# Performance work log

Measured on AMD Instinct MI355X. Metric: run time of the kernel, lower is better.

The kernel has to match this reference:

```python
import jax, jax.numpy as jnp
import numpy as np

B, T, C = 32, 128, 64
E, H = 8, 4            # feat_dim, num_heads
D = E // H             # head_dim = 2
HID = 32               # hidden_dim


def setup_inputs() -> dict:
    key = jax.random.key(0)
    ks = jax.random.split(key, 20)
    s = 0.1
    return {
        "x": jax.random.normal(ks[0], (B, T, C), jnp.float32),
        # input_proj: Linear(C, C)
        "W_in": jax.random.normal(ks[1], (C, C), jnp.float32) * s,
        "b_in": jax.random.normal(ks[2], (C,), jnp.float32) * s,
        # time_step_score: Linear(C, C//4) -> GELU -> Linear(C//4, 1) -> Sigmoid
        "W_ts1": jax.random.normal(ks[3], (C // 4, C), jnp.float32) * s,
        "b_ts1": jax.random.normal(ks[4], (C // 4,), jnp.float32) * s,
        "W_ts2": jax.random.normal(ks[5], (1, C // 4), jnp.float32) * s,
        "b_ts2": jax.random.normal(ks[6], (1,), jnp.float32) * s,
        # per-channel GRU(1 -> E): torch gate order (r, z, n)
        "W_ih": jax.random.normal(ks[7], (C, 3 * E), jnp.float32) * s,      # input size 1
        "W_hh": jax.random.normal(ks[8], (C, 3 * E, E), jnp.float32) * s,
        "b_ih": jax.random.normal(ks[9], (C, 3 * E), jnp.float32) * s,
        "b_hh": jax.random.normal(ks[10], (C, 3 * E), jnp.float32) * s,
        # shared MultiheadAttention(E, 4): packed in_proj + out_proj
        "W_qkv": jax.random.normal(ks[11], (3 * E, E), jnp.float32) * s,
        "b_qkv": jax.random.normal(ks[12], (3 * E,), jnp.float32) * s,
        "W_o": jax.random.normal(ks[13], (E, E), jnp.float32) * s,
        "b_o": jax.random.normal(ks[14], (E,), jnp.float32) * s,
        # out_proj: Linear(C*E, HID)
        "W_out": jax.random.normal(ks[15], (HID, C * E), jnp.float32) * s,
        "b_out": jax.random.normal(ks[16], (HID,), jnp.float32) * s,
    }


def _forward(x, W_in, b_in, W_ts1, b_ts1, W_ts2, b_ts2,
             W_ih, W_hh, b_ih, b_hh, W_qkv, b_qkv, W_o, b_o, W_out, b_out):
    bs, ts, c = x.shape
    # time step importance: per-timestep MLP over the raw features
    h1 = jax.nn.gelu(jnp.einsum('btc,fc->btf', x, W_ts1) + b_ts1, approximate=False)
    ts_imp = jax.nn.sigmoid(jnp.einsum('btf,of->bto', h1, W_ts2) + b_ts2)[..., 0]  # [B,T]

    xp = jnp.einsum('btc,dc->btd', x, W_in) + b_in  # [B,T,C]

    # Batched per-channel GRU scan over time. state h: [B,C,E]
    def step(h, x_t):
        gi = x_t[:, :, None] * W_ih[None] + b_ih          # [B,C,3E]
        gh = jnp.einsum('bce,cge->bcg', h, W_hh) + b_hh   # [B,C,3E]
        ir, iz, inn = gi[..., :E], gi[..., E:2 * E], gi[..., 2 * E:]
        hr, hz, hn = gh[..., :E], gh[..., E:2 * E], gh[..., 2 * E:]
        r = jax.nn.sigmoid(ir + hr)
        z = jax.nn.sigmoid(iz + hz)
        n = jnp.tanh(inn + r * hn)
        h_new = (1.0 - z) * n + z * h
        return h_new, h_new

    h0 = jnp.zeros((bs, c, E), xp.dtype)
    _, hs = jax.lax.scan(step, h0, jnp.transpose(xp, (1, 0, 2)))  # [T,B,C,E]
    hs_bcte = jnp.transpose(hs, (1, 2, 0, 3))                     # [B,C,T,E]

    # Shared MHA applied independently per channel (batched over B*C)
    qkv = jnp.einsum('bcte,fe->bctf', hs_bcte, W_qkv) + b_qkv     # [B,C,T,3E]
    q, k, v = qkv[..., :E], qkv[..., E:2 * E], qkv[..., 2 * E:]
    def heads(t):
        return t.reshape(bs, c, ts, H, D)
    q, k, v = heads(q), heads(k), heads(v)
    scores = jnp.einsum('bcthd,bcshd->bchts', q, k) / np.sqrt(D)
    attn = jax.nn.softmax(scores, axis=-1)
    o = jnp.einsum('bchts,bcshd->bcthd', attn, v).reshape(bs, c, ts, E)
    attn_out = jnp.einsum('bcte,fe->bctf', o, W_o) + b_o          # [B,C,T,E]
    attention = jnp.transpose(attn_out, (0, 2, 1, 3))             # [B,T,C,E]

    out_flat = jnp.transpose(hs, (1, 0, 2, 3)).reshape(bs, ts, c * E)  # [B,T,C*E]
    out = jnp.einsum('btf,hf->bth', out_flat, W_out) + b_out           # [B,T,HID]

    feat_imp = jax.nn.sigmoid(attention.sum(axis=(1, 3)))   # [B,C]
    tsf_imp = jax.nn.sigmoid(attention.sum(axis=-1))        # [B,T,C]
    return out[:, -1, :], feat_imp, ts_imp, tsf_imp


def reference(x, W_in, b_in, W_ts1, b_ts1, W_ts2, b_ts2,
              W_ih, W_hh, b_ih, b_hh, W_qkv, b_qkv, W_o, b_o, W_out, b_out):
    return _forward(x, W_in, b_in, W_ts1, b_ts1, W_ts2, b_ts2,
                    W_ih, W_hh, b_ih, b_hh, W_qkv, b_qkv, W_o, b_o, W_out, b_out)
```

## Files before the change

kernel.cpp:

```cpp
#include <hip/hip_runtime.h>
#include <hip/hip_bf16.h>
#include <math.h>

#define B_ 32
#define T_ 128
#define C_ 64
#define E_ 8
#define HID_ 32

#define LOG2E 1.44269504088896341f

__device__ __forceinline__ float fast_rcp(float x) { return __builtin_amdgcn_rcpf(x); }
__device__ __forceinline__ float fast_exp2(float x) { return exp2f(x); }
__device__ __forceinline__ float fast_sigmoid(float x) {
    return fast_rcp(1.0f + fast_exp2(-LOG2E * x));
}
__device__ __forceinline__ float fast_tanh(float x) {
    float xc = __builtin_amdgcn_fmed3f(x, -15.0f, 15.0f);
    float t = fast_exp2(2.0f * LOG2E * xc);
    return (t - 1.0f) * fast_rcp(t + 1.0f);
}

template <int CTRL>
__device__ __forceinline__ float dppf(float v) {
    return __int_as_float(__builtin_amdgcn_update_dpp(
        __float_as_int(v), __float_as_int(v), CTRL, 0xF, 0xF, false));
}
#define QP_XOR1 0xB1
#define QP_XOR2 0x4E
#define QP_XOR3 0x1B
#define HALF_MIRROR 0x141

__global__ __launch_bounds__(64) void k_pre_ts(
    const float* __restrict__ x, const float* __restrict__ W_in, const float* __restrict__ b_in,
    const float* __restrict__ W_ts1, const float* __restrict__ b_ts1,
    const float* __restrict__ W_ts2, const float* __restrict__ b_ts2,
    float* __restrict__ xp, float* __restrict__ ts_imp)
{
    const int bt = blockIdx.x;
    const int tid = threadIdx.x;
    __shared__ __align__(16) float xs[C_];
    __shared__ float h1[16];
    if (tid < 16) ((float4*)xs)[tid] = ((const float4*)(x + bt * C_))[tid];
    __syncthreads();

    float a = b_in[tid];
    const float4* w4 = (const float4*)(W_in + tid * C_);
#pragma unroll
    for (int k4 = 0; k4 < 16; ++k4) {
        float4 xv = ((const float4*)xs)[k4];
        float4 wv = w4[k4];
        a = fmaf(xv.x, wv.x, a); a = fmaf(xv.y, wv.y, a);
        a = fmaf(xv.z, wv.z, a); a = fmaf(xv.w, wv.w, a);
    }
    xp[bt * C_ + tid] = a;

    if (tid < 16) {
        float s = b_ts1[tid];
#pragma unroll
        for (int k = 0; k < C_; ++k) s = fmaf(xs[k], W_ts1[tid * C_ + k], s);
        h1[tid] = 0.5f * s * (1.0f + erff(s * 0.70710678118654752f));
    }
    __syncthreads();
    if (tid == 0) {
        float s = b_ts2[0];
#pragma unroll
        for (int k = 0; k < 16; ++k) s = fmaf(h1[k], W_ts2[k], s);
        ts_imp[bt] = fast_sigmoid(s);
    }
}

__global__ __launch_bounds__(64) void k_gru(
    const float* __restrict__ xp, const float* __restrict__ W_ih, const float* __restrict__ W_hh,
    const float* __restrict__ b_ih, const float* __restrict__ b_hh,
    float* __restrict__ hs, float* __restrict__ fh)
{
    const int tid = threadIdx.x;
    const int ci = tid >> 3;
    const int e = tid & 7;
    const int chain = blockIdx.x * 8 + ci;
    const int c = chain & 63;

    __shared__ float xc[8][T_ + 1];

    const int c_base = (blockIdx.x & 7) * 8;
    const int bb = blockIdx.x >> 3;
    for (int idx = tid; idx < 8 * T_; idx += 64) {
        int cci = idx & 7, t = idx >> 3;
        xc[cci][t] = xp[(bb * T_ + t) * C_ + c_base + cci];
    }
    __syncthreads();

    float wr[8], wz[8], wn[8];
#pragma unroll
    for (int m = 0; m < 8; ++m) {
        const int j = e ^ m;
        wr[m] = W_hh[(c * 24 + 0  + e) * 8 + j];
        wz[m] = W_hh[(c * 24 + 8  + e) * 8 + j];
        wn[m] = W_hh[(c * 24 + 16 + e) * 8 + j];
    }
    const float wir = W_ih[c * 24 + e], wiz = W_ih[c * 24 + 8 + e], win = W_ih[c * 24 + 16 + e];
    const float cr = b_ih[c * 24 + e] + b_hh[c * 24 + e];
    const float cz = b_ih[c * 24 + 8 + e] + b_hh[c * 24 + 8 + e];
    const float bin_ = b_ih[c * 24 + 16 + e];
    const float bhn  = b_hh[c * 24 + 16 + e];

    float h = 0.0f;
    float* ho = hs + (size_t)chain * T_ * E_ + e;
    float xv = xc[ci][0];
    for (int t = 0; t < T_; ++t) {
        float xvn = xc[ci][t + 1];
        float p1 = dppf<QP_XOR1>(h);
        float p2 = dppf<QP_XOR2>(h);
        float p3 = dppf<QP_XOR3>(h);
        float p7 = dppf<HALF_MIRROR>(h);
        float p6 = dppf<HALF_MIRROR>(p1);
        float p5 = dppf<HALF_MIRROR>(p2);
        float p4 = dppf<HALF_MIRROR>(p3);
        const float pa[8] = {h, p1, p2, p3, p4, p5, p6, p7};

        float g0 = fmaf(pa[1], wr[1], pa[0] * wr[0]);
        float g1 = fmaf(pa[3], wr[3], pa[2] * wr[2]);
        float g2 = fmaf(pa[5], wr[5], pa[4] * wr[4]);
        float g3 = fmaf(pa[7], wr[7], pa[6] * wr[6]);
        float gr = fmaf(xv, wir, cr) + ((g0 + g1) + (g2 + g3));
        float z0 = fmaf(pa[1], wz[1], pa[0] * wz[0]);
        float z1 = fmaf(pa[3], wz[3], pa[2] * wz[2]);
        float z2 = fmaf(pa[5], wz[5], pa[4] * wz[4]);
        float z3 = fmaf(pa[7], wz[7], pa[6] * wz[6]);
        float gz = fmaf(xv, wiz, cz) + ((z0 + z1) + (z2 + z3));
        float n0 = fmaf(pa[1], wn[1], pa[0] * wn[0]);
        float n1 = fmaf(pa[3], wn[3], pa[2] * wn[2]);
        float n2 = fmaf(pa[5], wn[5], pa[4] * wn[4]);
        float n3 = fmaf(pa[7], wn[7], pa[6] * wn[6]);
        float hn = bhn + ((n0 + n1) + (n2 + n3));
        float gn = fmaf(xv, win, bin_);
        float r = fast_sigmoid(gr);
        float z = fast_sigmoid(gz);
        float nn = fast_tanh(fmaf(r, hn, gn));
        h = fmaf(z, h - nn, nn);
        ho[t * E_] = h;
        xv = xvn;
    }
    fh[chain * E_ + e] = h;
}

__global__ __launch_bounds__(128) void k_qkvu(
    const float* __restrict__ hs, const float* __restrict__ W_qkv, const float* __restrict__ b_qkv,
    const float* __restrict__ W_o,
    float* __restrict__ kub)
{
    const int bc = blockIdx.x;
    const int s = threadIdx.x;
    const float4* hp = (const float4*)(hs + (size_t)bc * T_ * E_ + s * E_);
    float4 h0 = hp[0], h1 = hp[1];
    float hr[E_] = {h0.x, h0.y, h0.z, h0.w, h1.x, h1.y, h1.z, h1.w};

    float kv[E_];
#pragma unroll
    for (int f = 0; f < E_; ++f) {
        float a = b_qkv[E_ + f];
#pragma unroll
        for (int j = 0; j < E_; ++j) a = fmaf(hr[j], W_qkv[(E_ + f) * E_ + j], a);
        kv[f] = a;
    }
    float ws[E_];
#pragma unroll
    for (int d = 0; d < E_; ++d) {
        float wv = 0.0f;
#pragma unroll
        for (int fp = 0; fp < E_; ++fp) wv += W_o[fp * E_ + d];
        ws[d] = wv;
    }
    float vv[E_];
#pragma unroll
    for (int f = 0; f < E_; ++f) {
        float a = b_qkv[2 * E_ + f];
#pragma unroll
        for (int j = 0; j < E_; ++j) a = fmaf(hr[j], W_qkv[(2 * E_ + f) * E_ + j], a);
        vv[f] = a;
    }
    float4 uu;
    uu.x = fmaf(vv[1], ws[1], vv[0] * ws[0]);
    uu.y = fmaf(vv[3], ws[3], vv[2] * ws[2]);
    uu.z = fmaf(vv[5], ws[5], vv[4] * ws[4]);
    uu.w = fmaf(vv[7], ws[7], vv[6] * ws[6]);

    float4* rec = (float4*)(kub + ((size_t)bc * T_ + s) * 12);
    rec[0] = make_float4(kv[0], kv[1], kv[2], kv[3]);
    rec[1] = make_float4(kv[4], kv[5], kv[6], kv[7]);
    rec[2] = uu;
}

__global__ __launch_bounds__(128) void k_attn2(
    const float* __restrict__ hs, const float* __restrict__ W_qkv, const float* __restrict__ b_qkv,
    const float* __restrict__ b_o, const float* __restrict__ kub,
    float* __restrict__ feat_imp, float* __restrict__ tsf_imp)
{
    const int bc = blockIdx.x;
    const int b = bc >> 6, c = bc & 63;
    const int tid = threadIdx.x;
    const int w = tid >> 6;
    const int lane = tid & 63;
    const int row = tid;

    __shared__ float red2[2];

    const float qscale = 0.70710678118654752f * LOG2E;

    float q[E_];
    {
        const float4* hp = (const float4*)(hs + (size_t)bc * T_ * E_ + row * E_);
        float4 h0 = hp[0], h1 = hp[1];
        float hr[E_] = {h0.x, h0.y, h0.z, h0.w, h1.x, h1.y, h1.z, h1.w};
#pragma unroll
        for (int f = 0; f < E_; ++f) {
            float a = b_qkv[f];
#pragma unroll
            for (int j = 0; j < E_; ++j) a = fmaf(hr[j], W_qkv[f * E_ + j], a);
            q[f] = a * qscale;
        }
    }

    const float* kbase = kub + (size_t)bc * T_ * 12;
    float l[4] = {0.f, 0.f, 0.f, 0.f};
    float S[4] = {0.f, 0.f, 0.f, 0.f};
#pragma unroll 4
    for (int s = 0; s < T_; ++s) {
        const float4* r4 = (const float4*)(kbase + (size_t)s * 12);
        float4 ka = r4[0];
        float4 kb4 = r4[1];
        float4 uu = r4[2];
        float p0 = fast_exp2(fmaf(q[1], ka.y, q[0] * ka.x));
        float p1 = fast_exp2(fmaf(q[3], ka.w, q[2] * ka.z));
        float p2 = fast_exp2(fmaf(q[5], kb4.y, q[4] * kb4.x));
        float p3 = fast_exp2(fmaf(q[7], kb4.w, q[6] * kb4.z));
        l[0] += p0; l[1] += p1; l[2] += p2; l[3] += p3;
        S[0] = fmaf(p0, uu.x, S[0]);
        S[1] = fmaf(p1, uu.y, S[1]);
        S[2] = fmaf(p2, uu.z, S[2]);
        S[3] = fmaf(p3, uu.w, S[3]);
    }

    float bsum = 0.0f;
#pragma unroll
    for (int fp = 0; fp < E_; ++fp) bsum += b_o[fp];
    float Sv = bsum;
#pragma unroll
    for (int hh = 0; hh < 4; ++hh) Sv = fmaf(S[hh], fast_rcp(l[hh]), Sv);

    tsf_imp[(size_t)b * T_ * C_ + (size_t)row * C_ + c] = fast_sigmoid(Sv);

    float fsum = Sv;
#pragma unroll
    for (int off = 1; off <= 32; off <<= 1) fsum += __shfl_xor(fsum, off);
    if (lane == 0) red2[w] = fsum;
    __syncthreads();
    if (tid == 0) feat_imp[bc] = fast_sigmoid(red2[0] + red2[1]);
}

__global__ __launch_bounds__(128) void k_attn(
    const float* __restrict__ hs, const float* __restrict__ W_qkv, const float* __restrict__ b_qkv,
    const float* __restrict__ W_o, const float* __restrict__ b_o,
    float* __restrict__ feat_imp, float* __restrict__ tsf_imp)
{
    const int bc = blockIdx.x;
    const int b = bc >> 6, c = bc & 63;
    const int tid = threadIdx.x;
    const int w = tid >> 6;
    const int lane = tid & 63;
    const int ri = lane >> 1;
    const int sh = lane & 1;
    const int row0 = w * 64 + ri;
    const int row1 = w * 64 + 32 + ri;

    __shared__ __align__(16) float ks[2][516];
    __shared__ __align__(16) float us[2][260];
    __shared__ float qsT[E_][T_];
    __shared__ float red2[2];

    const float qscale = 0.70710678118654752f * LOG2E;

    {
        const int srow = tid;
        const float4* hp = (const float4*)(hs + (size_t)bc * T_ * E_ + srow * E_);
        float4 h0 = hp[0], h1 = hp[1];
        float hr[E_] = {h0.x, h0.y, h0.z, h0.w, h1.x, h1.y, h1.z, h1.w};
        float* kdst = &ks[srow >> 6][(srow & 63) * 8];
        float kv[E_];
#pragma unroll
        for (int f = 0; f < E_; ++f) {
            float a = b_qkv[E_ + f];
#pragma unroll
            for (int j = 0; j < E_; ++j) a = fmaf(hr[j], W_qkv[(E_ + f) * E_ + j], a);
            kv[f] = a;
        }
        ((float4*)kdst)[0] = make_float4(kv[0], kv[1], kv[2], kv[3]);
        ((float4*)kdst)[1] = make_float4(kv[4], kv[5], kv[6], kv[7]);
#pragma unroll
        for (int f = 0; f < E_; ++f) {
            float a = b_qkv[f];
#pragma unroll
            for (int j = 0; j < E_; ++j) a = fmaf(hr[j], W_qkv[f * E_ + j], a);
            qsT[f][srow] = a * qscale;
        }
        float ws[E_];
#pragma unroll
        for (int d = 0; d < E_; ++d) {
            float wv = 0.0f;
#pragma unroll
            for (int fp = 0; fp < E_; ++fp) wv += W_o[fp * E_ + d];
            ws[d] = wv;
        }
        float vv[E_];
#pragma unroll
        for (int f = 0; f < E_; ++f) {
            float a = b_qkv[2 * E_ + f];
#pragma unroll
            for (int j = 0; j < E_; ++j) a = fmaf(hr[j], W_qkv[(2 * E_ + f) * E_ + j], a);
            vv[f] = a;
        }
        float4 uu;
        uu.x = fmaf(vv[1], ws[1], vv[0] * ws[0]);
        uu.y = fmaf(vv[3], ws[3], vv[2] * ws[2]);
        uu.z = fmaf(vv[5], ws[5], vv[4] * ws[4]);
        uu.w = fmaf(vv[7], ws[7], vv[6] * ws[6]);
        *((float4*)&us[srow >> 6][(srow & 63) * 4]) = uu;
    }
    __syncthreads();

    float q0[E_], q1[E_];
#pragma unroll
    for (int f = 0; f < E_; ++f) { q0[f] = qsT[f][row0]; q1[f] = qsT[f][row1]; }

    float l0[4] = {0.f,0.f,0.f,0.f}, S0[4] = {0.f,0.f,0.f,0.f};
    float l1[4] = {0.f,0.f,0.f,0.f}, S1[4] = {0.f,0.f,0.f,0.f};
    const float* kb = &ks[sh][0];
    const float* ub = &us[sh][0];
#pragma unroll 8
    for (int i = 0; i < 64; ++i) {
        float4 k0 = *(const float4*)(kb + i * 8);
        float4 k1 = *(const float4*)(kb + i * 8 + 4);
        float4 uu = *(const float4*)(ub + i * 4);
        float p00 = fast_exp2(fmaf(q0[1], k0.y, q0[0] * k0.x));
        float p01 = fast_exp2(fmaf(q0[3], k0.w, q0[2] * k0.z));
        float p02 = fast_exp2(fmaf(q0[5], k1.y, q0[4] * k1.x));
        float p03 = fast_exp2(fmaf(q0[7], k1.w, q0[6] * k1.z));
        float p10 = fast_exp2(fmaf(q1[1], k0.y, q1[0] * k0.x));
        float p11 = fast_exp2(fmaf(q1[3], k0.w, q1[2] * k0.z));
        float p12 = fast_exp2(fmaf(q1[5], k1.y, q1[4] * k1.x));
        float p13 = fast_exp2(fmaf(q1[7], k1.w, q1[6] * k1.z));
        l0[0] += p00; l0[1] += p01; l0[2] += p02; l0[3] += p03;
        l1[0] += p10; l1[1] += p11; l1[2] += p12; l1[3] += p13;
        S0[0] = fmaf(p00, uu.x, S0[0]); S0[1] = fmaf(p01, uu.y, S0[1]);
        S0[2] = fmaf(p02, uu.z, S0[2]); S0[3] = fmaf(p03, uu.w, S0[3]);
        S1[0] = fmaf(p10, uu.x, S1[0]); S1[1] = fmaf(p11, uu.y, S1[1]);
        S1[2] = fmaf(p12, uu.z, S1[2]); S1[3] = fmaf(p13, uu.w, S1[3]);
    }

#pragma unroll
    for (int i = 0; i < 4; ++i) {
        l0[i] += __shfl_xor(l0[i], 1);  S0[i] += __shfl_xor(S0[i], 1);
        l1[i] += __shfl_xor(l1[i], 1);  S1[i] += __shfl_xor(S1[i], 1);
    }

    float bsum = 0.0f;
#pragma unroll
    for (int fp = 0; fp < E_; ++fp) bsum += b_o[fp];
    float Sa = bsum, Sb = bsum;
#pragma unroll
    for (int hh = 0; hh < 4; ++hh) {
        Sa = fmaf(S0[hh], fast_rcp(l0[hh]), Sa);
        Sb = fmaf(S1[hh], fast_rcp(l1[hh]), Sb);
    }

    if (sh == 0) {
        tsf_imp[(size_t)b * T_ * C_ + (size_t)row0 * C_ + c] = fast_sigmoid(Sa);
        tsf_imp[(size_t)b * T_ * C_ + (size_t)row1 * C_ + c] = fast_sigmoid(Sb);
    }

    float fsum = Sa + Sb;
#pragma unroll
    for (int off = 2; off <= 32; off <<= 1) fsum += __shfl_xor(fsum, off);
    if (lane == 0) red2[w] = fsum;
    __syncthreads();
    if (tid == 0) feat_imp[bc] = fast_sigmoid(red2[0] + red2[1]);
}

__global__ __launch_bounds__(64) void k_out(
    const float* __restrict__ fh, const float* __restrict__ W_out, const float* __restrict__ b_out,
    float* __restrict__ out0)
{
    const int b = blockIdx.x;
    const int tid = threadIdx.x;
    __shared__ float hf[C_ * E_];
    const float4* src = (const float4*)(fh + (b * C_ + tid) * E_);
    float4* dst = (float4*)(hf + tid * E_);
    dst[0] = src[0];
    dst[1] = src[1];
    __syncthreads();
    if (tid < HID_) {
        float a = b_out[tid];
        const float* wo = W_out + tid * (C_ * E_);
        for (int k = 0; k < C_ * E_; ++k) a = fmaf(hf[k], wo[k], a);
        out0[b * HID_ + tid] = a;
    }
}

extern "C" void kernel_launch(void* const* d_in, const int* in_sizes, int n_in,
                              void* d_out, int out_size, void* d_ws, size_t ws_size,
                              hipStream_t stream) {
    (void)in_sizes; (void)n_in; (void)out_size;

    float* out0 = (float*)d_out;
    float* feat = out0 + B_ * HID_;
    float* tsim = feat + B_ * C_;
    float* tsf  = tsim + B_ * T_;

    const float* x     = (const float*)d_in[0];
    const float* W_in  = (const float*)d_in[1];
    const float* b_in  = (const float*)d_in[2];
    const float* W_ts1 = (const float*)d_in[3];
    const float* b_ts1 = (const float*)d_in[4];
    const float* W_ts2 = (const float*)d_in[5];
    const float* b_ts2 = (const float*)d_in[6];
    const float* W_ih  = (const float*)d_in[7];
    const float* W_hh  = (const float*)d_in[8];
    const float* b_ih  = (const float*)d_in[9];
    const float* b_hh  = (const float*)d_in[10];
    const float* W_qkv = (const float*)d_in[11];
    const float* b_qkv = (const float*)d_in[12];
    const float* W_o   = (const float*)d_in[13];
    const float* b_o   = (const float*)d_in[14];
    const float* W_out = (const float*)d_in[15];
    const float* b_out = (const float*)d_in[16];

    float* fhb = (float*)d_ws;
    float* xpb = fhb + B_ * C_ * E_;
    float* hsb = xpb + (size_t)B_ * T_ * C_;
    float* kub = hsb + (size_t)B_ * C_ * T_ * E_;

    const size_t need = ((size_t)B_ * C_ * E_ + (size_t)B_ * T_ * C_ +
                         (size_t)B_ * C_ * T_ * E_ + (size_t)B_ * C_ * T_ * 12) * 4;

    hipLaunchKernelGGL(k_pre_ts, dim3(B_ * T_), dim3(64), 0, stream,
                       x, W_in, b_in, W_ts1, b_ts1, W_ts2, b_ts2, xpb, tsim);
    hipLaunchKernelGGL(k_gru, dim3(B_ * C_ / 8), dim3(64), 0, stream,
                       xpb, W_ih, W_hh, b_ih, b_hh, hsb, fhb);
    hipLaunchKernelGGL(k_out, dim3(B_), dim3(64), 0, stream,
                       fhb, W_out, b_out, out0);

    if (ws_size >= need) {
        hipLaunchKernelGGL(k_qkvu, dim3(B_ * C_), dim3(128), 0, stream,
                           hsb, W_qkv, b_qkv, W_o, kub);
        hipLaunchKernelGGL(k_attn2, dim3(B_ * C_), dim3(128), 0, stream,
                           hsb, W_qkv, b_qkv, b_o, kub, feat, tsf);
    } else {
        hipLaunchKernelGGL(k_attn, dim3(B_ * C_), dim3(128), 0, stream,
                           hsb, W_qkv, b_qkv, W_o, b_o, feat, tsf);
    }
}
```

Measured before the change: 106.2 us.

## Split attention kernel across heads with one wave per head

The attention-summary kernel now launches 512 threads per (batch, channel) block, with each wave owning one head for 64 query rows instead of each thread handling all four heads. Per-head partial results go to shared memory and are summed by the first 128 threads before the sigmoid outputs and the feature reduction. This raises parallelism and cuts per-thread serial work in the 128-step key loop. In exchange it adds a shared-memory stage, an extra barrier, and scalar loads that re-read each record once per head.

```diff
diff --git a/kernel.cpp b/kernel.cpp
--- a/kernel.cpp
+++ b/kernel.cpp
@@ -192,7 +192,7 @@
     rec[2] = uu;
 }
 
-__global__ __launch_bounds__(128) void k_attn2(
+__global__ __launch_bounds__(512) void k_attn3(
     const float* __restrict__ hs, const float* __restrict__ W_qkv, const float* __restrict__ b_qkv,
     const float* __restrict__ b_o, const float* __restrict__ kub,
     float* __restrict__ feat_imp, float* __restrict__ tsf_imp)
@@ -202,59 +202,56 @@
     const int tid = threadIdx.x;
     const int w = tid >> 6;
     const int lane = tid & 63;
-    const int row = tid;
-
+    const int head = __builtin_amdgcn_readfirstlane(w & 3);
+    const int row = (w >> 2) * 64 + lane;
+
+    __shared__ float sh[T_][5];
     __shared__ float red2[2];
 
     const float qscale = 0.70710678118654752f * LOG2E;
 
-    float q[E_];
+    float q0, q1;
     {
-        const float4* hp = (const float4*)(hs + (size_t)bc * T_ * E_ + row * E_);
+        const float4* hp = (const float4*)(hs + ((size_t)bc * T_ + row) * E_);
         float4 h0 = hp[0], h1 = hp[1];
         float hr[E_] = {h0.x, h0.y, h0.z, h0.w, h1.x, h1.y, h1.z, h1.w};
-#pragma unroll
-        for (int f = 0; f < E_; ++f) {
-            float a = b_qkv[f];
-#pragma unroll
-            for (int j = 0; j < E_; ++j) a = fmaf(hr[j], W_qkv[f * E_ + j], a);
-            q[f] = a * qscale;
+        float a0 = b_qkv[2 * head], a1 = b_qkv[2 * head + 1];
+#pragma unroll
+        for (int j = 0; j < E_; ++j) {
+            a0 = fmaf(hr[j], W_qkv[(2 * head) * E_ + j], a0);
+            a1 = fmaf(hr[j], W_qkv[(2 * head + 1) * E_ + j], a1);
         }
-    }
-
-    const float* kbase = kub + (size_t)bc * T_ * 12;
-    float l[4] = {0.f, 0.f, 0.f, 0.f};
-    float S[4] = {0.f, 0.f, 0.f, 0.f};
-#pragma unroll 4
+        q0 = a0 * qscale;
+        q1 = a1 * qscale;
+    }
+
+    const float* base = kub + (size_t)bc * T_ * 12;
+    float l = 0.0f, S = 0.0f;
+#pragma unroll 8
     for (int s = 0; s < T_; ++s) {
-        const float4* r4 = (const float4*)(kbase + (size_t)s * 12);
-        float4 ka = r4[0];
-        float4 kb4 = r4[1];
-        float4 uu = r4[2];
-        float p0 = fast_exp2(fmaf(q[1], ka.y, q[0] * ka.x));
-        float p1 = fast_exp2(fmaf(q[3], ka.w, q[2] * ka.z));
-        float p2 = fast_exp2(fmaf(q[5], kb4.y, q[4] * kb4.x));
-        float p3 = fast_exp2(fmaf(q[7], kb4.w, q[6] * kb4.z));
-        l[0] += p0; l[1] += p1; l[2] += p2; l[3] += p3;
-        S[0] = fmaf(p0, uu.x, S[0]);
-        S[1] = fmaf(p1, uu.y, S[1]);
-        S[2] = fmaf(p2, uu.z, S[2]);
-        S[3] = fmaf(p3, uu.w, S[3]);
-    }
-
-    float bsum = 0.0f;
-#pragma unroll
-    for (int fp = 0; fp < E_; ++fp) bsum += b_o[fp];
-    float Sv = bsum;
-#pragma unroll
-    for (int hh = 0; hh < 4; ++hh) Sv = fmaf(S[hh], fast_rcp(l[hh]), Sv);
-
-    tsf_imp[(size_t)b * T_ * C_ + (size_t)row * C_ + c] = fast_sigmoid(Sv);
-
-    float fsum = Sv;
-#pragma unroll
-    for (int off = 1; off <= 32; off <<= 1) fsum += __shfl_xor(fsum, off);
-    if (lane == 0) red2[w] = fsum;
+        const float* rec = base + s * 12;
+        float k0 = rec[2 * head];
+        float k1 = rec[2 * head + 1];
+        float u  = rec[8 + head];
+        float p = fast_exp2(fmaf(q1, k1, q0 * k0));
+        l += p;
+        S = fmaf(p, u, S);
+    }
+    sh[row][head] = S * fast_rcp(l);
+    __syncthreads();
+
+    if (tid < T_) {
+        const int r = tid;
+        float bsum = 0.0f;
+#pragma unroll
+        for (int fp = 0; fp < E_; ++fp) bsum += b_o[fp];
+        float Sv = bsum + ((sh[r][0] + sh[r][1]) + (sh[r][2] + sh[r][3]));
+        tsf_imp[(size_t)b * T_ * C_ + (size_t)r * C_ + c] = fast_sigmoid(Sv);
+        float fsum = Sv;
+#pragma unroll
+        for (int off = 1; off <= 32; off <<= 1) fsum += __shfl_xor(fsum, off);
+        if ((tid & 63) == 0) red2[tid >> 6] = fsum;
+    }
     __syncthreads();
     if (tid == 0) feat_imp[bc] = fast_sigmoid(red2[0] + red2[1]);
 }
@@ -453,7 +450,7 @@
     if (ws_size >= need) {
         hipLaunchKernelGGL(k_qkvu, dim3(B_ * C_), dim3(128), 0, stream,
                            hsb, W_qkv, b_qkv, W_o, kub);
-        hipLaunchKernelGGL(k_attn2, dim3(B_ * C_), dim3(128), 0, stream,
+        hipLaunchKernelGGL(k_attn3, dim3(B_ * C_), dim3(512), 0, stream,
                            hsb, W_qkv, b_qkv, b_o, kub, feat, tsf);
     } else {
         hipLaunchKernelGGL(k_attn, dim3(B_ * C_), dim3(128), 0, stream,
```

After: 103.1 us. -2.9%, faster.
